# Kernel tuning notes

Hardware: AMD Instinct MI355X
Metric: run time of the kernel (lower is better)

The kernel has to match this reference:

```python
import jax, jax.numpy as jnp
import numpy as np

C = 32          # in/out channels per spnn.Conv3d(32, 32, 2, stride=2)
KVOL = 8        # 2^3 kernel offsets
GRID = 128      # voxel grid resolution
N_RAW = 1_000_000


def setup_inputs() -> dict:
    rng = np.random.default_rng(0)
    # unique active voxel coordinates (torchsparse coords are unique)
    coords = np.unique(rng.integers(0, GRID, size=(N_RAW, 3), dtype=np.int32), axis=0)
    n = coords.shape[0]
    # kernel=2, stride=2: each input voxel hits exactly one output voxel
    out_coords = coords // 2
    k_idx = (coords[:, 0] % 2) * 4 + (coords[:, 1] % 2) * 2 + (coords[:, 2] % 2)
    _, out_idx = np.unique(out_coords, axis=0, return_inverse=True)
    num_out = int(out_idx.max()) + 1

    key = jax.random.key(0)
    kx, kw = jax.random.split(key)
    x = jax.random.normal(kx, (n, C), dtype=jnp.float32)
    W = jax.random.normal(kw, (KVOL, C, C), dtype=jnp.float32) * 0.05
    return {
        "x": x,
        "W": W,
        "k_idx": jnp.asarray(k_idx, dtype=jnp.int32),
        "out_idx": jnp.asarray(out_idx, dtype=jnp.int32),
        "num_out": num_out,
    }


def reference(x, W, k_idx, out_idx, num_out):
    # gather -> per-offset GEMM -> scatter-add (sparse conv kernel-map form)
    # proj[n, k, d] = sum_c x[n, c] * W[k, c, d]
    proj = jnp.einsum("nc,kcd->nkd", x, W)
    # pick the projection for each point's kernel offset: [n, C]
    sel = jnp.take_along_axis(proj, k_idx[:, None, None], axis=1)[:, 0, :]
    # scatter-add into output voxels
    out = jax.ops.segment_sum(sel, out_idx, num_segments=num_out)
    return out
```

## Files before the change

kernel.cpp:

```cpp
#include <hip/hip_runtime.h>
#include <hip/hip_bf16.h>


typedef __attribute__((ext_vector_type(8))) short bf16x8;
typedef __attribute__((ext_vector_type(4))) float f32x4;

union ABFrag { bf16x8 v; int i[4]; };
union BFI { __hip_bfloat162 h; int i; };

__device__ __forceinline__ int pack2_bf16(float a, float b) {
    BFI u; u.h = __float22bfloat162_rn(make_float2(a, b));
    return u.i;
}

__device__ __forceinline__ unsigned short f2bf(float f) {
    union { float f; unsigned u; } v; v.f = f;
    unsigned r = v.u + 0x7FFFu + ((v.u >> 16) & 1u);
    return (unsigned short)(r >> 16);
}

__global__ __launch_bounds__(256) void prep_fill_kernel(
    const float* __restrict__ W, unsigned short* __restrict__ WB,
    int4* __restrict__ child4, int n4) {
    int t = blockIdx.x * blockDim.x + threadIdx.x;
    if (t < 8 * 2 * 64 * 8) {
        int j    = t & 7;
        int lane = (t >> 3) & 63;
        int half = (t >> 9) & 1;
        int k    = t >> 10;
        int c = (lane >> 4) * 8 + j;
        int d = half * 16 + (lane & 15);
        WB[t] = f2bf(W[k * 1024 + c * 32 + d]);
    }
    const int4 m1 = make_int4(-1, -1, -1, -1);
    for (int i = t; i < n4; i += gridDim.x * blockDim.x) child4[i] = m1;
}

__global__ __launch_bounds__(256) void convert_build_kernel(
    const float4* __restrict__ x4, int2* __restrict__ xb2,
    const int* __restrict__ k_idx, const int* __restrict__ out_idx,
    int* __restrict__ child, int n) {
    int t = blockIdx.x * blockDim.x + threadIdx.x;
    if (t < n) child[(size_t)out_idx[t] * 8 + k_idx[t]] = t;
    const int n4 = n * 8;
    const int stride = gridDim.x * blockDim.x;
    for (int i = t; i < n4; i += stride) {
        float4 v = x4[i];
        xb2[i] = make_int2(pack2_bf16(v.x, v.y), pack2_bf16(v.z, v.w));
    }
}

__global__ __launch_bounds__(256, 4) void conv_gather_kernel(
    const unsigned short* __restrict__ xb,
    const unsigned short* __restrict__ WB,
    const int* __restrict__ child,
    float* __restrict__ out,
    int num_out)
{
    const int lane  = threadIdx.x & 63;
    const int wv    = threadIdx.x >> 6;
    const int obase = (blockIdx.x * 4 + wv) * 16;
    if (obase >= num_out) return;

    const int row  = lane & 15;
    const int quad = lane >> 4;
    int o = obase + row;
    if (o >= num_out) o = num_out - 1;

    const int4* cp = (const int4*)(child + (size_t)o * 8);
    int4 c0 = cp[0], c1 = cp[1];
    int pk[8] = {c0.x, c0.y, c0.z, c0.w, c1.x, c1.y, c1.z, c1.w};

    bf16x8 xr[8];
#pragma unroll
    for (int k = 0; k < 8; ++k) {
        int p = pk[k] < 0 ? 0 : pk[k];
        xr[k] = *(const bf16x8*)(xb + (size_t)p * 32 + quad * 8);
    }

    f32x4 acc0 = {0.f, 0.f, 0.f, 0.f};
    f32x4 acc1 = {0.f, 0.f, 0.f, 0.f};

#pragma unroll
    for (int k = 0; k < 8; ++k) {
        const bool valid = pk[k] >= 0;
        ABFrag a; a.v = xr[k];
        a.i[0] = valid ? a.i[0] : 0;
        a.i[1] = valid ? a.i[1] : 0;
        a.i[2] = valid ? a.i[2] : 0;
        a.i[3] = valid ? a.i[3] : 0;
        bf16x8 b0 = *(const bf16x8*)(WB + ((size_t)(k * 2 + 0) * 64 + lane) * 8);
        bf16x8 b1 = *(const bf16x8*)(WB + ((size_t)(k * 2 + 1) * 64 + lane) * 8);
        acc0 = __builtin_amdgcn_mfma_f32_16x16x32_bf16(a.v, b0, acc0, 0, 0, 0);
        acc1 = __builtin_amdgcn_mfma_f32_16x16x32_bf16(a.v, b1, acc1, 0, 0, 0);
    }

#pragma unroll
    for (int r = 0; r < 4; ++r) {
        int oo = obase + quad * 4 + r;
        if (oo < num_out) {
            float* op = out + (size_t)oo * 32 + (lane & 15);
            op[0]  = acc0[r];
            op[16] = acc1[r];
        }
    }
}

__global__ void prep_w_kernel(const float* __restrict__ W,
                              unsigned short* __restrict__ WB) {
    int t = blockIdx.x * blockDim.x + threadIdx.x;
    if (t >= 8 * 2 * 64 * 8) return;
    int j = t & 7, lane = (t >> 3) & 63, half = (t >> 9) & 1, k = t >> 10;
    int c = (lane >> 4) * 8 + j;
    int d = half * 16 + (lane & 15);
    WB[t] = f2bf(W[k * 1024 + c * 32 + d]);
}

__global__ __launch_bounds__(256) void conv_atomic_kernel(
    const float* __restrict__ x, const unsigned short* __restrict__ WB,
    const int* __restrict__ k_idx, const int* __restrict__ out_idx,
    float* __restrict__ out, int n)
{
    const int lane = threadIdx.x & 63;
    const int wv   = threadIdx.x >> 6;
    const int base = (blockIdx.x * 4 + wv) * 16;
    if (base >= n) return;
    const int row = lane & 15, quad = lane >> 4;
    const int p = base + row;
    int krow = -1;
    ABFrag a; a.i[0] = a.i[1] = a.i[2] = a.i[3] = 0;
    if (p < n) {
        krow = k_idx[p];
        const float* xp = x + (size_t)p * 32 + quad * 8;
        float4 x0 = *(const float4*)xp;
        float4 x1 = *(const float4*)(xp + 4);
        a.i[0] = pack2_bf16(x0.x, x0.y);
        a.i[1] = pack2_bf16(x0.z, x0.w);
        a.i[2] = pack2_bf16(x1.x, x1.y);
        a.i[3] = pack2_bf16(x1.z, x1.w);
    }
    f32x4 acc0 = {0.f,0.f,0.f,0.f}, acc1 = {0.f,0.f,0.f,0.f};
#pragma unroll
    for (int k = 0; k < 8; ++k) {
        bf16x8 b0 = *(const bf16x8*)(WB + ((size_t)(k*2+0)*64 + lane)*8);
        bf16x8 b1 = *(const bf16x8*)(WB + ((size_t)(k*2+1)*64 + lane)*8);
        const bool keep = (krow == k);
        ABFrag ak;
        ak.i[0] = keep ? a.i[0] : 0; ak.i[1] = keep ? a.i[1] : 0;
        ak.i[2] = keep ? a.i[2] : 0; ak.i[3] = keep ? a.i[3] : 0;
        acc0 = __builtin_amdgcn_mfma_f32_16x16x32_bf16(ak.v, b0, acc0, 0, 0, 0);
        acc1 = __builtin_amdgcn_mfma_f32_16x16x32_bf16(ak.v, b1, acc1, 0, 0, 0);
    }
#pragma unroll
    for (int r = 0; r < 4; ++r) {
        int p2 = base + quad * 4 + r;
        if (p2 < n) {
            int oi = out_idx[p2];
            float* op = out + (size_t)oi * 32 + (lane & 15);
            atomicAdd(op,      acc0[r]);
            atomicAdd(op + 16, acc1[r]);
        }
    }
}

extern "C" void kernel_launch(void* const* d_in, const int* in_sizes, int n_in,
                              void* d_out, int out_size, void* d_ws, size_t ws_size,
                              hipStream_t stream) {
    const float* x       = (const float*)d_in[0];
    const float* W       = (const float*)d_in[1];
    const int*   k_idx   = (const int*)d_in[2];
    const int*   out_idx = (const int*)d_in[3];
    const int n = in_sizes[2];
    const int num_out = out_size / 32;
    float* out = (float*)d_out;

    unsigned short* WB = (unsigned short*)d_ws;
    const size_t wb_bytes = 16384;
    int* child = (int*)((char*)d_ws + wb_bytes);
    const size_t child_bytes = (size_t)num_out * 8 * sizeof(int);
    size_t xb_off = wb_bytes + ((child_bytes + 255) & ~(size_t)255);
    unsigned short* xb = (unsigned short*)((char*)d_ws + xb_off);
    const size_t xb_bytes = (size_t)n * 32 * sizeof(unsigned short);

    if (ws_size >= xb_off + xb_bytes) {
        int n4 = num_out * 2;
        int blocksA = (n4 + 255) / 256;
        if (blocksA < 32) blocksA = 32;
        prep_fill_kernel<<<blocksA, 256, 0, stream>>>(W, WB, (int4*)child, n4);
        convert_build_kernel<<<(n + 255) / 256, 256, 0, stream>>>(
            (const float4*)x, (int2*)xb, k_idx, out_idx, child, n);
        int blocks = (num_out + 63) / 64;
        conv_gather_kernel<<<blocks, 256, 0, stream>>>(xb, WB, child, out, num_out);
    } else {
        prep_w_kernel<<<32, 256, 0, stream>>>(W, WB);
        hipMemsetAsync(d_out, 0, (size_t)out_size * sizeof(float), stream);
        int blocks = (n + 63) / 64;
        conv_atomic_kernel<<<blocks, 256, 0, stream>>>(x, WB, k_idx, out_idx, out, n);
    }
}
```

Before: 193.4 us.

## Process two 16-voxel tiles per wave in a persistent grid-stride gather kernel

The gather conv kernel now has each wave handle 32 output voxels as two 16-row MFMA tiles, reusing the loaded weight fragments for both. It also becomes a persistent kernel with at most 768 blocks looping over 128-voxel tiles. The goal is more gather loads in flight per wave and less per-block launch and weight-load overhead. The cost is doubled register use, which is why launch bounds drop to 3 blocks per CU, so occupancy may fall.

```diff
diff --git a/kernel.cpp b/kernel.cpp
--- a/kernel.cpp
+++ b/kernel.cpp
@@ -50,58 +50,77 @@
     }
 }
 
-__global__ __launch_bounds__(256, 4) void conv_gather_kernel(
+__global__ __launch_bounds__(256, 3) void conv_gather_kernel(
     const unsigned short* __restrict__ xb,
     const unsigned short* __restrict__ WB,
     const int* __restrict__ child,
     float* __restrict__ out,
-    int num_out)
+    int num_out, int nTiles)
 {
-    const int lane  = threadIdx.x & 63;
-    const int wv    = threadIdx.x >> 6;
-    const int obase = (blockIdx.x * 4 + wv) * 16;
-    if (obase >= num_out) return;
-
+    const int lane = threadIdx.x & 63;
+    const int wv   = threadIdx.x >> 6;
     const int row  = lane & 15;
     const int quad = lane >> 4;
-    int o = obase + row;
-    if (o >= num_out) o = num_out - 1;
-
-    const int4* cp = (const int4*)(child + (size_t)o * 8);
-    int4 c0 = cp[0], c1 = cp[1];
-    int pk[8] = {c0.x, c0.y, c0.z, c0.w, c1.x, c1.y, c1.z, c1.w};
-
-    bf16x8 xr[8];
-#pragma unroll
-    for (int k = 0; k < 8; ++k) {
-        int p = pk[k] < 0 ? 0 : pk[k];
-        xr[k] = *(const bf16x8*)(xb + (size_t)p * 32 + quad * 8);
-    }
-
-    f32x4 acc0 = {0.f, 0.f, 0.f, 0.f};
-    f32x4 acc1 = {0.f, 0.f, 0.f, 0.f};
-
-#pragma unroll
-    for (int k = 0; k < 8; ++k) {
-        const bool valid = pk[k] >= 0;
-        ABFrag a; a.v = xr[k];
-        a.i[0] = valid ? a.i[0] : 0;
-        a.i[1] = valid ? a.i[1] : 0;
-        a.i[2] = valid ? a.i[2] : 0;
-        a.i[3] = valid ? a.i[3] : 0;
-        bf16x8 b0 = *(const bf16x8*)(WB + ((size_t)(k * 2 + 0) * 64 + lane) * 8);
-        bf16x8 b1 = *(const bf16x8*)(WB + ((size_t)(k * 2 + 1) * 64 + lane) * 8);
-        acc0 = __builtin_amdgcn_mfma_f32_16x16x32_bf16(a.v, b0, acc0, 0, 0, 0);
-        acc1 = __builtin_amdgcn_mfma_f32_16x16x32_bf16(a.v, b1, acc1, 0, 0, 0);
-    }
-
-#pragma unroll
-    for (int r = 0; r < 4; ++r) {
-        int oo = obase + quad * 4 + r;
-        if (oo < num_out) {
-            float* op = out + (size_t)oo * 32 + (lane & 15);
-            op[0]  = acc0[r];
-            op[16] = acc1[r];
+
+    for (int t = blockIdx.x; t < nTiles; t += gridDim.x) {
+        const int obase = t * 128 + wv * 32;
+
+        int oA = obase + row;        if (oA >= num_out) oA = num_out - 1;
+        int oB = obase + 16 + row;   if (oB >= num_out) oB = num_out - 1;
+        const int4* cA = (const int4*)(child + (size_t)oA * 8);
+        const int4* cB = (const int4*)(child + (size_t)oB * 8);
+        int4 ca0 = cA[0], ca1 = cA[1];
+        int4 cb0 = cB[0], cb1 = cB[1];
+        int pkA[8] = {ca0.x, ca0.y, ca0.z, ca0.w, ca1.x, ca1.y, ca1.z, ca1.w};
+        int pkB[8] = {cb0.x, cb0.y, cb0.z, cb0.w, cb1.x, cb1.y, cb1.z, cb1.w};
+
+        bf16x8 xrA[8], xrB[8];
+#pragma unroll
+        for (int k = 0; k < 8; ++k) {
+            int p = pkA[k] < 0 ? 0 : pkA[k];
+            xrA[k] = *(const bf16x8*)(xb + (size_t)p * 32 + quad * 8);
+        }
+#pragma unroll
+        for (int k = 0; k < 8; ++k) {
+            int p = pkB[k] < 0 ? 0 : pkB[k];
+            xrB[k] = *(const bf16x8*)(xb + (size_t)p * 32 + quad * 8);
+        }
+
+        f32x4 accA0 = {0.f,0.f,0.f,0.f}, accA1 = {0.f,0.f,0.f,0.f};
+        f32x4 accB0 = {0.f,0.f,0.f,0.f}, accB1 = {0.f,0.f,0.f,0.f};
+
+#pragma unroll
+        for (int k = 0; k < 8; ++k) {
+            bf16x8 w0 = *(const bf16x8*)(WB + ((size_t)(k * 2 + 0) * 64 + lane) * 8);
+            bf16x8 w1 = *(const bf16x8*)(WB + ((size_t)(k * 2 + 1) * 64 + lane) * 8);
+            ABFrag aA; aA.v = xrA[k];
+            bool vA = pkA[k] >= 0;
+            aA.i[0] = vA ? aA.i[0] : 0;  aA.i[1] = vA ? aA.i[1] : 0;
+            aA.i[2] = vA ? aA.i[2] : 0;  aA.i[3] = vA ? aA.i[3] : 0;
+            ABFrag aB; aB.v = xrB[k];
+            bool vB = pkB[k] >= 0;
+            aB.i[0] = vB ? aB.i[0] : 0;  aB.i[1] = vB ? aB.i[1] : 0;
+            aB.i[2] = vB ? aB.i[2] : 0;  aB.i[3] = vB ? aB.i[3] : 0;
+            accA0 = __builtin_amdgcn_mfma_f32_16x16x32_bf16(aA.v, w0, accA0, 0, 0, 0);
+            accA1 = __builtin_amdgcn_mfma_f32_16x16x32_bf16(aA.v, w1, accA1, 0, 0, 0);
+            accB0 = __builtin_amdgcn_mfma_f32_16x16x32_bf16(aB.v, w0, accB0, 0, 0, 0);
+            accB1 = __builtin_amdgcn_mfma_f32_16x16x32_bf16(aB.v, w1, accB1, 0, 0, 0);
+        }
+
+#pragma unroll
+        for (int r = 0; r < 4; ++r) {
+            int vA = obase + quad * 4 + r;
+            if (vA < num_out) {
+                float* op = out + (size_t)vA * 32 + row;
+                op[0]  = accA0[r];
+                op[16] = accA1[r];
+            }
+            int vB = obase + 16 + quad * 4 + r;
+            if (vB < num_out) {
+                float* op = out + (size_t)vB * 32 + row;
+                op[0]  = accB0[r];
+                op[16] = accB1[r];
+            }
         }
     }
 }
@@ -189,8 +208,10 @@
         prep_fill_kernel<<<blocksA, 256, 0, stream>>>(W, WB, (int4*)child, n4);
         convert_build_kernel<<<(n + 255) / 256, 256, 0, stream>>>(
             (const float4*)x, (int2*)xb, k_idx, out_idx, child, n);
-        int blocks = (num_out + 63) / 64;
-        conv_gather_kernel<<<blocks, 256, 0, stream>>>(xb, WB, child, out, num_out);
+        int nTiles = (num_out + 127) / 128;
+        int blocks = nTiles < 768 ? nTiles : 768;
+        conv_gather_kernel<<<blocks, 256, 0, stream>>>(xb, WB, child, out,
+                                                       num_out, nTiles);
     } else {
         prep_w_kernel<<<32, 256, 0, stream>>>(W, WB);
         hipMemsetAsync(d_out, 0, (size_t)out_size * sizeof(float), stream);
```

New measurement: 189.5 us. 1.02x faster.
